# Kernel optimization log

Hardware: AMD Instinct MI355X
Metric: run time of the kernel (lower is better)

## Reference

```python
import jax, jax.numpy as jnp
import numpy as np

N, S, E = 8, 1024, 768
H = 12
D = E // H  # head_dim = 64
FF = 4 * E
EPS = 1e-5


def setup_inputs() -> dict:
    key = jax.random.key(0)
    ks = jax.random.split(key, 12)
    s = lambda fan_in: 1.0 / np.sqrt(fan_in)
    return {
        "x": jax.random.normal(ks[0], (N, S, E), dtype=jnp.float32),
        "ln1_g": jnp.ones((E,), jnp.float32),
        "ln1_b": jnp.zeros((E,), jnp.float32),
        "ln2_g": jnp.ones((E,), jnp.float32),
        "ln2_b": jnp.zeros((E,), jnp.float32),
        "w_attn": jax.random.normal(ks[1], (E, 3 * E), jnp.float32) * s(E),
        "b_attn": jax.random.normal(ks[2], (3 * E,), jnp.float32) * 0.02,
        "w_proj": jax.random.normal(ks[3], (E, E), jnp.float32) * s(E),
        "b_proj": jax.random.normal(ks[4], (E,), jnp.float32) * 0.02,
        "w_fc": jax.random.normal(ks[5], (E, FF), jnp.float32) * s(E),
        "b_fc": jax.random.normal(ks[6], (FF,), jnp.float32) * 0.02,
        "w_fc2": jax.random.normal(ks[7], (FF, E), jnp.float32) * s(FF),
        "b_fc2": jax.random.normal(ks[8], (E,), jnp.float32) * 0.02,
    }


def _layernorm(x, g, b):
    mu = jnp.mean(x, axis=-1, keepdims=True)
    var = jnp.var(x, axis=-1, keepdims=True)
    return (x - mu) * jax.lax.rsqrt(var + EPS) * g + b


def reference(x, ln1_g, ln1_b, ln2_g, ln2_b, w_attn, b_attn, w_proj, b_proj,
              w_fc, b_fc, w_fc2, b_fc2):
    # --- attention branch (pre-LN) ---
    h = _layernorm(x, ln1_g, ln1_b)
    qkv = h @ w_attn + b_attn                       # [N,S,3E]
    q, k, v = jnp.split(qkv, 3, axis=-1)
    q = q.reshape(N, S, H, D).transpose(0, 2, 1, 3)  # [N,H,S,D]
    k = k.reshape(N, S, H, D).transpose(0, 2, 1, 3)
    v = v.reshape(N, S, H, D).transpose(0, 2, 1, 3)
    attn = jnp.einsum('nhsd,nhtd->nhst', q, k) * (1.0 / np.sqrt(D))
    causal = jnp.tril(jnp.ones((S, S), bool))
    attn = jnp.where(causal, attn, -jnp.inf)
    p = jax.nn.softmax(attn, axis=-1)
    out = jnp.einsum('nhst,nhtd->nhsd', p, v)        # [N,H,S,D]
    out = out.transpose(0, 2, 1, 3).reshape(N, S, E)
    x = x + (out @ w_proj + b_proj)
    # --- MLP branch ---
    h2 = _layernorm(x, ln2_g, ln2_b)
    ff = jax.nn.gelu(h2 @ w_fc + b_fc, approximate=False)  # exact GELU (torch nn.GELU default)
    x = x + (ff @ w_fc2 + b_fc2)
    return x
```

## Files before the change

kernel.cpp:

```cpp
#include <hip/hip_runtime.h>
#include <hip/hip_bf16.h>
#include <stdint.h>

#define S_LEN 1024
#define E_DIM 768
#define H_N   12
#define FF_DIM 3072

typedef __hip_bfloat16 bf16;
using short8  = __attribute__((ext_vector_type(8))) short;
using short4v = __attribute__((ext_vector_type(4))) short;
using f32x4   = __attribute__((ext_vector_type(4))) float;

__device__ __forceinline__ void async_cp16(const void* g, void* l) {
  __builtin_amdgcn_global_load_lds(
      (__attribute__((address_space(1))) void*)(g),
      (__attribute__((address_space(3))) void*)(l), 16, 0, 0);
}

__global__ __launch_bounds__(256) void wcastT_all(
    const float* __restrict__ wa, const float* __restrict__ wp,
    const float* __restrict__ wf, const float* __restrict__ wf2,
    bf16* __restrict__ oa, bf16* __restrict__ op,
    bf16* __restrict__ of, bf16* __restrict__ of2) {
  __shared__ float t[32][33];
  int bid = blockIdx.x;
  const float* w; bf16* wt; int K, N, bx, by;
  if (bid < 1728)      { w = wa;  wt = oa;  K = 768;  N = 2304; int r = bid;        bx = r % 72; by = r / 72; }
  else if (bid < 2304) { w = wp;  wt = op;  K = 768;  N = 768;  int r = bid - 1728; bx = r % 24; by = r / 24; }
  else if (bid < 4608) { w = wf;  wt = of;  K = 768;  N = 3072; int r = bid - 2304; bx = r % 96; by = r / 96; }
  else                 { w = wf2; wt = of2; K = 3072; N = 768;  int r = bid - 4608; bx = r % 24; by = r / 24; }
  int x = threadIdx.x & 31;
  int y = threadIdx.x >> 5;
  for (int i = y; i < 32; i += 8)
    t[i][x] = w[(size_t)(by * 32 + i) * N + bx * 32 + x];
  __syncthreads();
  for (int i = y; i < 32; i += 8)
    wt[(size_t)(bx * 32 + i) * K + by * 32 + x] = __float2bfloat16(t[x][i]);
}

__global__ __launch_bounds__(256) void ln_rows(const float* __restrict__ x,
                                               const float* __restrict__ g,
                                               const float* __restrict__ b,
                                               bf16* __restrict__ out) {
  int row = blockIdx.x;
  int tid = threadIdx.x;
  const float* xr = x + (size_t)row * E_DIM;
  float v0 = xr[tid], v1 = xr[tid + 256], v2 = xr[tid + 512];
  float s = v0 + v1 + v2;
  float ss = v0 * v0 + v1 * v1 + v2 * v2;
  for (int o = 32; o > 0; o >>= 1) {
    s  += __shfl_down(s, o);
    ss += __shfl_down(ss, o);
  }
  __shared__ float ps[4], pq[4];
  int wv = tid >> 6;
  if ((tid & 63) == 0) { ps[wv] = s; pq[wv] = ss; }
  __syncthreads();
  s  = ps[0] + ps[1] + ps[2] + ps[3];
  ss = pq[0] + pq[1] + pq[2] + pq[3];
  float mu  = s * (1.0f / E_DIM);
  float var = ss * (1.0f / E_DIM) - mu * mu;
  float rs  = rsqrtf(var + 1e-5f);
  bf16* orow = out + (size_t)row * E_DIM;
  orow[tid]       = __float2bfloat16((v0 - mu) * rs * g[tid]       + b[tid]);
  orow[tid + 256] = __float2bfloat16((v1 - mu) * rs * g[tid + 256] + b[tid + 256]);
  orow[tid + 512] = __float2bfloat16((v2 - mu) * rs * g[tid + 512] + b[tid + 512]);
}

template <int MODE>
__global__ __launch_bounds__(512, 2) void gemm8(
    const bf16* __restrict__ A, const bf16* __restrict__ Bt,
    const float* __restrict__ bias,
    bf16* __restrict__ ob0, bf16* __restrict__ ob1, bf16* __restrict__ ob2,
    int M, int N, int K) {
  __shared__ bf16 lA[2][16384];
  __shared__ bf16 lB[2][16384];
  int tid = threadIdx.x;
  int w = tid >> 6, lane = tid & 63;
  int quad = lane >> 4, l16 = lane & 15;
  int wr = w >> 2, wc = w & 3;
  int gx = N >> 8;
  int flat = blockIdx.x;
  int y8 = flat & 7;
  int q2 = flat >> 3;
  int bx = q2 % gx;
  int by = (q2 / gx) * 8 + y8;
  int m0 = by << 8, n0 = bx << 8;

  f32x4 acc[8][4];
#pragma unroll
  for (int i = 0; i < 8; i++)
#pragma unroll
    for (int j = 0; j < 4; j++)
#pragma unroll
      for (int r = 0; r < 4; r++) acc[i][j][r] = 0.f;

  int xs = l16 & 7;
  int ko0 = (quad ^ xs) << 3;
  int ko1 = ((4 + quad) ^ xs) << 3;
  int sgo = ((tid & 7) ^ ((tid >> 3) & 7)) << 3;
  size_t aRB = (size_t)(m0 + (tid >> 3)) * K + sgo;
  size_t bRB = (size_t)(n0 + ((tid >> 8) << 6) + ((tid >> 3) & 31)) * K + sgo;
  int aD = tid * 8;
  int bD = ((tid >> 8) << 12) + (tid & 255) * 8;

  auto stA = [&](int buf, int mh, int kt) {
#pragma unroll
    for (int p = 0; p < 2; ++p)
      async_cp16(A + aRB + (size_t)(mh * 64 + p * 128) * K + (size_t)kt * 64,
                 &lA[buf][aD + mh * 4096 + p * 8192]);
  };
  auto stB = [&](int buf, int nh, int kt) {
#pragma unroll
    for (int p = 0; p < 2; ++p)
      async_cp16(Bt + bRB + (size_t)(nh * 32 + p * 128) * K + (size_t)kt * 64,
                 &lB[buf][bD + nh * 2048 + p * 8192]);
  };

  short8 af[4][2], b0f[2][2], b1f[2][2];

#define LD_A(BUF, MH)                                                      \
  {                                                                        \
    _Pragma("unroll") for (int i = 0; i < 4; ++i) {                        \
      const bf16* bp = &lA[BUF][(wr * 128 + (MH)*64 + i * 16 + l16) * 64]; \
      af[i][0] = *(const short8*)&bp[ko0];                                 \
      af[i][1] = *(const short8*)&bp[ko1];                                 \
    }                                                                      \
  }
#define LD_B(BUF, NH, DST)                                                 \
  {                                                                        \
    _Pragma("unroll") for (int j = 0; j < 2; ++j) {                        \
      const bf16* bp = &lB[BUF][(wc * 64 + (NH)*32 + j * 16 + l16) * 64];  \
      DST[j][0] = *(const short8*)&bp[ko0];                                \
      DST[j][1] = *(const short8*)&bp[ko1];                                \
    }                                                                      \
  }
#define DO_MFMA(MH, NH, BSRC)                                              \
  {                                                                        \
    __builtin_amdgcn_s_setprio(1);                                         \
    _Pragma("unroll") for (int ks = 0; ks < 2; ++ks)                       \
        _Pragma("unroll") for (int i = 0; i < 4; ++i)                      \
            _Pragma("unroll") for (int j = 0; j < 2; ++j)                  \
                acc[(MH)*4 + i][(NH)*2 + j] =                              \
        __builtin_amdgcn_mfma_f32_16x16x32_bf16(                           \
            BSRC[j][ks], af[i][ks], acc[(MH)*4 + i][(NH)*2 + j], 0, 0, 0); \
    __builtin_amdgcn_s_setprio(0);                                         \
  }
#define BAR() __builtin_amdgcn_s_barrier()
#define LGKM0() asm volatile("s_waitcnt lgkmcnt(0)" ::: "memory")
#define VM6() asm volatile("s_waitcnt vmcnt(6)" ::: "memory")
#define VM0() asm volatile("s_waitcnt vmcnt(0)" ::: "memory")

  stA(0, 0, 0); stA(0, 1, 0); stB(0, 0, 0); stB(0, 1, 0);
  stA(1, 0, 1); stB(1, 1, 1); stA(1, 1, 1);
  VM6();
  BAR();

  int nit = K >> 7;
  for (int it = 0; it < nit; ++it) {
    int kt1 = 2 * it + 1, ktA = 2 * it + 2, ktB = 2 * it + 3;
    bool more = (it + 1 < nit);
    LD_A(0, 0); LD_B(0, 0, b0f);
    stB(1, 0, kt1);
    BAR(); LGKM0(); DO_MFMA(0, 0, b0f); BAR();
    LD_B(0, 1, b1f);
    if (more) stA(0, 0, ktA);
    BAR(); LGKM0(); DO_MFMA(0, 1, b1f); BAR();
    LD_A(0, 1);
    if (more) stB(0, 1, ktA);
    BAR(); LGKM0(); DO_MFMA(1, 1, b1f); BAR();
    LD_B(0, 0, b0f);
    if (more) { stA(0, 1, ktA); VM6(); } else { VM0(); }
    BAR(); LGKM0(); DO_MFMA(1, 0, b0f); BAR();
    LD_A(1, 0); LD_B(1, 0, b0f);
    if (more) stB(0, 0, ktA);
    BAR(); LGKM0(); DO_MFMA(0, 0, b0f); BAR();
    LD_B(1, 1, b1f);
    if (more) stA(1, 0, ktB);
    BAR(); LGKM0(); DO_MFMA(0, 1, b1f); BAR();
    LD_A(1, 1);
    if (more) stB(1, 1, ktB);
    BAR(); LGKM0(); DO_MFMA(1, 1, b1f); BAR();
    LD_B(1, 0, b0f);
    if (more) { stA(1, 1, ktB); VM6(); }
    BAR(); LGKM0(); DO_MFMA(1, 0, b0f); BAR();
  }

#pragma unroll
  for (int nj = 0; nj < 4; ++nj) {
    int colb = n0 + wc * 64 + nj * 16 + quad * 4;
    f32x4 b4 = *(const f32x4*)&bias[colb];
#pragma unroll
    for (int mi = 0; mi < 8; ++mi) {
      int row = m0 + wr * 128 + mi * 16 + l16;
      f32x4 v = acc[mi][nj] + b4;
      if (MODE == 0) {
        int nn = row >> 10, s = row & 1023;
        if (colb < 768) {
          int h = colb >> 6, db = colb & 63;
          short4v pk;
          for (int r = 0; r < 4; r++)
            pk[r] = __builtin_bit_cast(short, __float2bfloat16(v[r] * 0.125f));
          *(short4v*)&ob0[(((size_t)nn * H_N + h) * S_LEN + s) * 64 + db] = pk;
        } else if (colb < 1536) {
          int c = colb - 768;
          size_t nh2 = (size_t)nn * H_N + (c >> 6);
          int d = c & 63;
          short4v pk;
          for (int r = 0; r < 4; r++)
            pk[r] = __builtin_bit_cast(short, __float2bfloat16(v[r]));
          *(short4v*)&ob1[((nh2 * 8 + (d >> 3)) * S_LEN + s) * 8 + (d & 7)] = pk;
        } else {
          int c = colb - 1536;
          size_t nh2 = (size_t)nn * H_N + (c >> 6);
          int d0 = c & 63;
          for (int r = 0; r < 4; r++)
            ob2[((nh2 * 128 + (s >> 3)) * 64 + d0 + r) * 8 + (s & 7)] =
                __float2bfloat16(v[r]);
        }
      } else if (MODE == 2) {
        short4v pk;
        for (int r = 0; r < 4; r++) {
          float x = v[r];
          float t = x * (1.59576912161f + 0.0713548162726f * x * x);
          float g = x * __builtin_amdgcn_rcpf(1.0f + __expf(-t));
          pk[r] = __builtin_bit_cast(short, __float2bfloat16(g));
        }
        *(short4v*)&ob0[(size_t)row * N + colb] = pk;
      }
    }
  }
#undef LD_A
#undef LD_B
#undef DO_MFMA
#undef BAR
#undef LGKM0
#undef VM6
#undef VM0
}

__global__ __launch_bounds__(256) void gemm_bt64(
    const bf16* __restrict__ A, const bf16* __restrict__ Bt,
    const float* __restrict__ bias, const float* __restrict__ resid,
    float* __restrict__ outf, int M, int N, int K) {
  __shared__ bf16 As[2][128 * 64];
  __shared__ bf16 Bs[2][64 * 64];
  int tid = threadIdx.x;
  int wave = tid >> 6, lane = tid & 63;
  int quad = lane >> 4, l16 = lane & 15;
  int gx = N >> 6;
  int flat = blockIdx.x;
  int y8 = flat & 7;
  int q2 = flat >> 3;
  int bx = q2 % gx;
  int by = (q2 / gx) * 8 + y8;
  int m0 = by * 128, n0 = bx * 64;
  int wm = wave * 32;
  f32x4 acc[2][4];
  for (int i = 0; i < 2; i++)
    for (int j = 0; j < 4; j++)
      for (int r = 0; r < 4; r++) acc[i][j][r] = 0.f;

  int xs = l16 & 7;
  int srow = tid >> 3;
  int scg = (((tid & 7) ^ (srow & 7)) << 3);
  const bf16* aptr = A  + (size_t)(m0 + srow) * K + scg;
  const bf16* bptr = Bt + (size_t)(n0 + srow) * K + scg;
  int ldst = tid * 8;

#pragma unroll
  for (int t = 0; t < 4; t++)
    async_cp16(aptr + (size_t)t * 32 * K, &As[0][ldst + t * 2048]);
#pragma unroll
  for (int t = 0; t < 2; t++)
    async_cp16(bptr + (size_t)t * 32 * K, &Bs[0][ldst + t * 2048]);

  int nkb = K >> 6;
  for (int ik = 0; ik < nkb; ++ik) {
    int cur = ik & 1;
    if (ik + 1 < nkb) {
      size_t ko = (size_t)(ik + 1) * 64;
#pragma unroll
      for (int t = 0; t < 4; t++)
        async_cp16(aptr + ko + (size_t)t * 32 * K, &As[cur ^ 1][ldst + t * 2048]);
#pragma unroll
      for (int t = 0; t < 2; t++)
        async_cp16(bptr + ko + (size_t)t * 32 * K, &Bs[cur ^ 1][ldst + t * 2048]);
      asm volatile("s_waitcnt vmcnt(6)" ::: "memory");
    } else {
      asm volatile("s_waitcnt vmcnt(0)" ::: "memory");
    }
    __builtin_amdgcn_s_barrier();
    asm volatile("" ::: "memory");
#pragma unroll
    for (int ks = 0; ks < 2; ks++) {
      int ko2 = (((ks * 4 + quad) ^ xs) << 3);
      short8 af[2], bfr[4];
      for (int i = 0; i < 2; i++)
        af[i] = *(const short8*)&As[cur][(wm + i * 16 + l16) * 64 + ko2];
      for (int j = 0; j < 4; j++)
        bfr[j] = *(const short8*)&Bs[cur][(j * 16 + l16) * 64 + ko2];
      for (int i = 0; i < 2; i++)
        for (int j = 0; j < 4; j++)
          acc[i][j] = __builtin_amdgcn_mfma_f32_16x16x32_bf16(
              bfr[j], af[i], acc[i][j], 0, 0, 0);
    }
    asm volatile("" ::: "memory");
    __builtin_amdgcn_s_barrier();
  }

  for (int j = 0; j < 4; j++) {
    int colb = n0 + j * 16 + quad * 4;
    f32x4 b4 = *(const f32x4*)&bias[colb];
    for (int i = 0; i < 2; i++) {
      int row = m0 + wm + i * 16 + l16;
      size_t idx = (size_t)row * N + colb;
      f32x4 rv = *(const f32x4*)&resid[idx];
      *(f32x4*)&outf[idx] = acc[i][j] + b4 + rv;
    }
  }
}

__global__ __launch_bounds__(256) void attn_fwd(
    const bf16* __restrict__ q, const bf16* __restrict__ kg,
    const bf16* __restrict__ vg, bf16* __restrict__ out) {
  __shared__ bf16 kt2[2][8 * 64 * 8];
  __shared__ bf16 vt2[2][8 * 64 * 8];
  __shared__ bf16 pba[4][16 * 68];
  __shared__ bf16 pbb[4][16 * 68];
  int flat = blockIdx.x;
  int xcd = flat & 7;
  int j = flat >> 3;
  int a = j & 7;
  int g = j >> 3;
  int nh = xcd * 12 + g;
  int b = 15 - a;
  int n = nh / H_N, h = nh % H_N;
  int tid = threadIdx.x, wave = tid >> 6, lane = tid & 63;
  int quad = lane >> 4, l16 = lane & 15;
  const bf16* qp = q  + (size_t)nh * S_LEN * 64;
  const bf16* kp = kg + (size_t)nh * 8 * S_LEN * 8;
  const bf16* vp = vg + (size_t)nh * 128 * 64 * 8;
  int qra = a * 64 + wave * 16;
  int qrb = b * 64 + wave * 16;

  short8 qfa[2], qfb[2];
  qfa[0] = *(const short8*)&qp[(size_t)(qra + l16) * 64 + quad * 8];
  qfa[1] = *(const short8*)&qp[(size_t)(qra + l16) * 64 + 32 + quad * 8];
  qfb[0] = *(const short8*)&qp[(size_t)(qrb + l16) * 64 + quad * 8];
  qfb[1] = *(const short8*)&qp[(size_t)(qrb + l16) * 64 + 32 + quad * 8];

  const bf16* kbase = kp + (((size_t)(tid >> 6) * S_LEN) + (tid & 63)) * 8;
  const bf16* vbase = vp + (((size_t)(tid >> 6) * 64) + (tid & 63)) * 8;

  f32x4 oaa[4], oab[4];
  for (int dt = 0; dt < 4; dt++)
    for (int r = 0; r < 4; r++) { oaa[dt][r] = 0.f; oab[dt][r] = 0.f; }
  float lia = 0.f, lib = 0.f;

  {
    bf16* lk = &kt2[0][0] + tid * 8;
    bf16* lv = &vt2[0][0] + tid * 8;
#pragma unroll
    for (int t = 0; t < 2; ++t) {
      async_cp16(kbase + (size_t)t * 4 * S_LEN * 8, lk + t * 2048);
      async_cp16(vbase + (size_t)t * 2048, lv + t * 2048);
    }
  }

  for (int kb = 0; kb <= b; ++kb) {
    bool act_a = (kb <= a);
    int cur = kb & 1;
    __syncthreads();

    short8 kf[2][4], vf[2][4];
#pragma unroll
    for (int ks = 0; ks < 2; ks++)
      for (int nt = 0; nt < 4; nt++) {
        kf[ks][nt] = *(const short8*)
            &kt2[cur][(size_t)((ks * 4 + quad) * 64 + nt * 16 + l16) * 8];
        vf[ks][nt] = *(const short8*)
            &vt2[cur][(size_t)((ks * 4 + quad) * 64 + nt * 16 + l16) * 8];
      }
    if (kb < b) {
      bf16* lk = &kt2[cur ^ 1][0] + tid * 8;
      bf16* lv = &vt2[cur ^ 1][0] + tid * 8;
      size_t kko = (size_t)(kb + 1) * 512;
      size_t vko = (size_t)(kb + 1) * 4096;
#pragma unroll
      for (int t = 0; t < 2; ++t) {
        async_cp16(kbase + kko + (size_t)t * 4 * S_LEN * 8, lk + t * 2048);
        async_cp16(vbase + vko + (size_t)t * 2048, lv + t * 2048);
      }
    }

    f32x4 sb4[4], sa4[4];
    for (int nt = 0; nt < 4; nt++) {
      for (int r = 0; r < 4; r++) { sb4[nt][r] = -10.f; sa4[nt][r] = -10.f; }
      for (int ks = 0; ks < 2; ks++) {
        sb4[nt] = __builtin_amdgcn_mfma_f32_16x16x32_bf16(kf[ks][nt], qfb[ks],
                                                          sb4[nt], 0, 0, 0);
        if (act_a)
          sa4[nt] = __builtin_amdgcn_mfma_f32_16x16x32_bf16(kf[ks][nt], qfa[ks],
                                                            sa4[nt], 0, 0, 0);
      }
    }
    if (kb == b) {
      int ql = wave * 16 + l16;
      for (int nt = 0; nt < 4; nt++)
        for (int r = 0; r < 4; r++)
          if (nt * 16 + quad * 4 + r > ql) sb4[nt][r] = -INFINITY;
    }
    if (kb == a) {
      int ql = wave * 16 + l16;
      for (int nt = 0; nt < 4; nt++)
        for (int r = 0; r < 4; r++)
          if (nt * 16 + quad * 4 + r > ql) sa4[nt][r] = -INFINITY;
    }

    float rsb = 0.f;
    for (int nt = 0; nt < 4; nt++)
      for (int r = 0; r < 4; r++) {
        float p = __expf(sb4[nt][r]);
        sb4[nt][r] = p;
        rsb += p;
      }
    rsb += __shfl_xor(rsb, 16);
    rsb += __shfl_xor(rsb, 32);
    lib += rsb;
    bf16* pwb = pbb[wave];
    for (int nt = 0; nt < 4; nt++) {
      short4v pk;
      for (int r = 0; r < 4; r++)
        pk[r] = __builtin_bit_cast(short, __float2bfloat16(sb4[nt][r]));
      *(short4v*)&pwb[l16 * 68 + nt * 16 + quad * 4] = pk;
    }
    if (act_a) {
      float rsa = 0.f;
      for (int nt = 0; nt < 4; nt++)
        for (int r = 0; r < 4; r++) {
          float p = __expf(sa4[nt][r]);
          sa4[nt][r] = p;
          rsa += p;
        }
      rsa += __shfl_xor(rsa, 16);
      rsa += __shfl_xor(rsa, 32);
      lia += rsa;
      bf16* pwa = pba[wave];
      for (int nt = 0; nt < 4; nt++) {
        short4v pk;
        for (int r = 0; r < 4; r++)
          pk[r] = __builtin_bit_cast(short, __float2bfloat16(sa4[nt][r]));
        *(short4v*)&pwa[l16 * 68 + nt * 16 + quad * 4] = pk;
      }
    }
    asm volatile("s_waitcnt lgkmcnt(0)" ::: "memory");

    for (int ks = 0; ks < 2; ks++) {
      short8 pfb = *(const short8*)&pbb[wave][l16 * 68 + ks * 32 + quad * 8];
      short8 pfa;
      if (act_a) pfa = *(const short8*)&pba[wave][l16 * 68 + ks * 32 + quad * 8];
      for (int dt = 0; dt < 4; dt++) {
        oab[dt] = __builtin_amdgcn_mfma_f32_16x16x32_bf16(vf[ks][dt], pfb,
                                                          oab[dt], 0, 0, 0);
        if (act_a)
          oaa[dt] = __builtin_amdgcn_mfma_f32_16x16x32_bf16(vf[ks][dt], pfa,
                                                            oaa[dt], 0, 0, 0);
      }
    }
  }

  float inva = 1.0f / lia, invb = 1.0f / lib;
  int ta = n * S_LEN + qra + l16;
  int tb = n * S_LEN + qrb + l16;
  for (int dt = 0; dt < 4; dt++) {
    short4v ova, ovb;
    for (int r = 0; r < 4; r++) {
      ova[r] = __builtin_bit_cast(short, __float2bfloat16(oaa[dt][r] * inva));
      ovb[r] = __builtin_bit_cast(short, __float2bfloat16(oab[dt][r] * invb));
    }
    *(short4v*)&out[(size_t)ta * E_DIM + h * 64 + dt * 16 + quad * 4] = ova;
    *(short4v*)&out[(size_t)tb * E_DIM + h * 64 + dt * 16 + quad * 4] = ovb;
  }
}

extern "C" void kernel_launch(void* const* d_in, const int* in_sizes, int n_in,
                              void* d_out, int out_size, void* d_ws, size_t ws_size,
                              hipStream_t stream) {
  (void)in_sizes; (void)n_in; (void)out_size; (void)ws_size;
  const float* x      = (const float*)d_in[0];
  const float* ln1_g  = (const float*)d_in[1];
  const float* ln1_b  = (const float*)d_in[2];
  const float* ln2_g  = (const float*)d_in[3];
  const float* ln2_b  = (const float*)d_in[4];
  const float* w_attn = (const float*)d_in[5];
  const float* b_attn = (const float*)d_in[6];
  const float* w_proj = (const float*)d_in[7];
  const float* b_proj = (const float*)d_in[8];
  const float* w_fc   = (const float*)d_in[9];
  const float* b_fc   = (const float*)d_in[10];
  const float* w_fc2  = (const float*)d_in[11];
  const float* b_fc2  = (const float*)d_in[12];
  float* out = (float*)d_out;

  char* ws = (char*)d_ws;
  bf16* wt_attn = (bf16*)(ws);
  bf16* wt_proj = (bf16*)(ws + 3538944);
  bf16* wt_fc   = (bf16*)(ws + 4718592);
  bf16* wt_fc2  = (bf16*)(ws + 9437184);
  bf16* hbuf    = (bf16*)(ws + 14155776);
  float* x2     = (float*)(ws + 26738688);
  bf16* qb      = (bf16*)(ws + 51904512);
  bf16* kbuf    = (bf16*)(ws + 64487424);
  bf16* vtb     = (bf16*)(ws + 77070336);
  bf16* ao      = (bf16*)(ws + 89653248);
  bf16* ff      = qb;

  dim3 blk(256);
  wcastT_all<<<dim3(6912), blk, 0, stream>>>(w_attn, w_proj, w_fc, w_fc2,
                                             wt_attn, wt_proj, wt_fc, wt_fc2);

  ln_rows<<<8192, blk, 0, stream>>>(x, ln1_g, ln1_b, hbuf);

  gemm8<0><<<dim3(288), dim3(512), 0, stream>>>(
      hbuf, wt_attn, b_attn, qb, kbuf, vtb, 8192, 2304, 768);

  attn_fwd<<<dim3(768), blk, 0, stream>>>(qb, kbuf, vtb, ao);

  gemm_bt64<<<dim3(12 * 64), blk, 0, stream>>>(
      ao, wt_proj, b_proj, x, x2, 8192, 768, 768);

  ln_rows<<<8192, blk, 0, stream>>>(x2, ln2_g, ln2_b, hbuf);

  gemm8<2><<<dim3(384), dim3(512), 0, stream>>>(
      hbuf, wt_fc, b_fc, ff, nullptr, nullptr, 8192, 3072, 768);

  gemm_bt64<<<dim3(12 * 64), blk, 0, stream>>>(
      ff, wt_fc2, b_fc2, x2, out, 8192, 768, 3072);
}
```

Before: 367.5 us.

## Write QKV GEMM output row-major and scatter V in separate kernel

The QKV GEMM epilogue now writes a plain row-major [tokens, 2304] bf16 buffer instead of scattering Q, K and V into per-head layouts. Attention reads Q and K straight from that strided buffer. A new scatter_v kernel rebuilds the blocked transposed V layout the attention kernel needs. The aim is to remove the scattered, partly scalar stores in the GEMM epilogue, at the cost of an extra kernel launch, an extra pass over V, and strided K/Q loads inside attention.

```diff
diff --git a/kernel.cpp b/kernel.cpp
--- a/kernel.cpp
+++ b/kernel.cpp
@@ -68,11 +68,26 @@
   orow[tid + 512] = __float2bfloat16((v2 - mu) * rs * g[tid + 512] + b[tid + 512]);
 }
 
+__global__ __launch_bounds__(256) void scatter_v(const bf16* __restrict__ qkv,
+                                                 bf16* __restrict__ vtb) {
+  int blk = blockIdx.x;
+  int n = blk >> 7, soct = blk & 127;
+  int tid = threadIdx.x;
+  for (int j = tid; j < 768; j += 256) {
+    int h = j >> 6, d = j & 63;
+    const bf16* src = qkv + ((size_t)(n * 1024 + soct * 8)) * 2304 + 1536 + h * 64 + d;
+    short8 v;
+#pragma unroll
+    for (int i = 0; i < 8; i++)
+      v[i] = __builtin_bit_cast(short, src[(size_t)i * 2304]);
+    *(short8*)&vtb[((((size_t)n * 12 + h) * 128 + soct) * 64 + d) * 8] = v;
+  }
+}
+
 template <int MODE>
 __global__ __launch_bounds__(512, 2) void gemm8(
     const bf16* __restrict__ A, const bf16* __restrict__ Bt,
-    const float* __restrict__ bias,
-    bf16* __restrict__ ob0, bf16* __restrict__ ob1, bf16* __restrict__ ob2,
+    const float* __restrict__ bias, bf16* __restrict__ outb,
     int M, int N, int K) {
   __shared__ bf16 lA[2][16384];
   __shared__ bf16 lB[2][16384];
@@ -191,44 +206,24 @@
   for (int nj = 0; nj < 4; ++nj) {
     int colb = n0 + wc * 64 + nj * 16 + quad * 4;
     f32x4 b4 = *(const f32x4*)&bias[colb];
+    float sc = (MODE == 1 && colb < 768) ? 0.125f : 1.0f;
 #pragma unroll
     for (int mi = 0; mi < 8; ++mi) {
       int row = m0 + wr * 128 + mi * 16 + l16;
       f32x4 v = acc[mi][nj] + b4;
-      if (MODE == 0) {
-        int nn = row >> 10, s = row & 1023;
-        if (colb < 768) {
-          int h = colb >> 6, db = colb & 63;
-          short4v pk;
-          for (int r = 0; r < 4; r++)
-            pk[r] = __builtin_bit_cast(short, __float2bfloat16(v[r] * 0.125f));
-          *(short4v*)&ob0[(((size_t)nn * H_N + h) * S_LEN + s) * 64 + db] = pk;
-        } else if (colb < 1536) {
-          int c = colb - 768;
-          size_t nh2 = (size_t)nn * H_N + (c >> 6);
-          int d = c & 63;
-          short4v pk;
-          for (int r = 0; r < 4; r++)
-            pk[r] = __builtin_bit_cast(short, __float2bfloat16(v[r]));
-          *(short4v*)&ob1[((nh2 * 8 + (d >> 3)) * S_LEN + s) * 8 + (d & 7)] = pk;
-        } else {
-          int c = colb - 1536;
-          size_t nh2 = (size_t)nn * H_N + (c >> 6);
-          int d0 = c & 63;
-          for (int r = 0; r < 4; r++)
-            ob2[((nh2 * 128 + (s >> 3)) * 64 + d0 + r) * 8 + (s & 7)] =
-                __float2bfloat16(v[r]);
-        }
-      } else if (MODE == 2) {
-        short4v pk;
+      short4v pk;
+      if (MODE == 1) {
+        for (int r = 0; r < 4; r++)
+          pk[r] = __builtin_bit_cast(short, __float2bfloat16(v[r] * sc));
+      } else {
         for (int r = 0; r < 4; r++) {
           float x = v[r];
           float t = x * (1.59576912161f + 0.0713548162726f * x * x);
           float g = x * __builtin_amdgcn_rcpf(1.0f + __expf(-t));
           pk[r] = __builtin_bit_cast(short, __float2bfloat16(g));
         }
-        *(short4v*)&ob0[(size_t)row * N + colb] = pk;
-      }
+      }
+      *(short4v*)&outb[(size_t)row * N + colb] = pk;
     }
   }
 #undef LD_A
@@ -323,8 +318,8 @@
 }
 
 __global__ __launch_bounds__(256) void attn_fwd(
-    const bf16* __restrict__ q, const bf16* __restrict__ kg,
-    const bf16* __restrict__ vg, bf16* __restrict__ out) {
+    const bf16* __restrict__ qkv, const bf16* __restrict__ vg,
+    bf16* __restrict__ out) {
   __shared__ bf16 kt2[2][8 * 64 * 8];
   __shared__ bf16 vt2[2][8 * 64 * 8];
   __shared__ bf16 pba[4][16 * 68];
@@ -339,19 +334,19 @@
   int n = nh / H_N, h = nh % H_N;
   int tid = threadIdx.x, wave = tid >> 6, lane = tid & 63;
   int quad = lane >> 4, l16 = lane & 15;
-  const bf16* qp = q  + (size_t)nh * S_LEN * 64;
-  const bf16* kp = kg + (size_t)nh * 8 * S_LEN * 8;
+  const bf16* qp = qkv + (size_t)n * S_LEN * 2304 + (size_t)h * 64;
   const bf16* vp = vg + (size_t)nh * 128 * 64 * 8;
   int qra = a * 64 + wave * 16;
   int qrb = b * 64 + wave * 16;
 
   short8 qfa[2], qfb[2];
-  qfa[0] = *(const short8*)&qp[(size_t)(qra + l16) * 64 + quad * 8];
-  qfa[1] = *(const short8*)&qp[(size_t)(qra + l16) * 64 + 32 + quad * 8];
-  qfb[0] = *(const short8*)&qp[(size_t)(qrb + l16) * 64 + quad * 8];
-  qfb[1] = *(const short8*)&qp[(size_t)(qrb + l16) * 64 + 32 + quad * 8];
-
-  const bf16* kbase = kp + (((size_t)(tid >> 6) * S_LEN) + (tid & 63)) * 8;
+  qfa[0] = *(const short8*)&qp[(size_t)(qra + l16) * 2304 + quad * 8];
+  qfa[1] = *(const short8*)&qp[(size_t)(qra + l16) * 2304 + 32 + quad * 8];
+  qfb[0] = *(const short8*)&qp[(size_t)(qrb + l16) * 2304 + quad * 8];
+  qfb[1] = *(const short8*)&qp[(size_t)(qrb + l16) * 2304 + 32 + quad * 8];
+
+  const bf16* kbase = qkv + ((size_t)n * S_LEN + (tid & 63)) * 2304 + 768 +
+                      h * 64 + ((tid >> 6) << 3);
   const bf16* vbase = vp + (((size_t)(tid >> 6) * 64) + (tid & 63)) * 8;
 
   f32x4 oaa[4], oab[4];
@@ -364,7 +359,7 @@
     bf16* lv = &vt2[0][0] + tid * 8;
 #pragma unroll
     for (int t = 0; t < 2; ++t) {
-      async_cp16(kbase + (size_t)t * 4 * S_LEN * 8, lk + t * 2048);
+      async_cp16(kbase + t * 32, lk + t * 2048);
       async_cp16(vbase + (size_t)t * 2048, lv + t * 2048);
     }
   }
@@ -386,11 +381,11 @@
     if (kb < b) {
       bf16* lk = &kt2[cur ^ 1][0] + tid * 8;
       bf16* lv = &vt2[cur ^ 1][0] + tid * 8;
-      size_t kko = (size_t)(kb + 1) * 512;
+      size_t kko = (size_t)(kb + 1) * 64 * 2304;
       size_t vko = (size_t)(kb + 1) * 4096;
 #pragma unroll
       for (int t = 0; t < 2; ++t) {
-        async_cp16(kbase + kko + (size_t)t * 4 * S_LEN * 8, lk + t * 2048);
+        async_cp16(kbase + kko + t * 32, lk + t * 2048);
         async_cp16(vbase + vko + (size_t)t * 2048, lv + t * 2048);
       }
     }
@@ -511,11 +506,10 @@
   bf16* wt_fc2  = (bf16*)(ws + 9437184);
   bf16* hbuf    = (bf16*)(ws + 14155776);
   float* x2     = (float*)(ws + 26738688);
-  bf16* qb      = (bf16*)(ws + 51904512);
-  bf16* kbuf    = (bf16*)(ws + 64487424);
-  bf16* vtb     = (bf16*)(ws + 77070336);
-  bf16* ao      = (bf16*)(ws + 89653248);
-  bf16* ff      = qb;
+  bf16* qkvb    = (bf16*)(ws + 51904512);
+  bf16* vtb     = (bf16*)(ws + 89653248);
+  bf16* ao      = hbuf;
+  bf16* ff      = qkvb;
 
   dim3 blk(256);
   wcastT_all<<<dim3(6912), blk, 0, stream>>>(w_attn, w_proj, w_fc, w_fc2,
@@ -523,10 +517,12 @@
 
   ln_rows<<<8192, blk, 0, stream>>>(x, ln1_g, ln1_b, hbuf);
 
-  gemm8<0><<<dim3(288), dim3(512), 0, stream>>>(
-      hbuf, wt_attn, b_attn, qb, kbuf, vtb, 8192, 2304, 768);
-
-  attn_fwd<<<dim3(768), blk, 0, stream>>>(qb, kbuf, vtb, ao);
+  gemm8<1><<<dim3(288), dim3(512), 0, stream>>>(
+      hbuf, wt_attn, b_attn, qkvb, 8192, 2304, 768);
+
+  scatter_v<<<dim3(1024), blk, 0, stream>>>(qkvb, vtb);
+
+  attn_fwd<<<dim3(768), blk, 0, stream>>>(qkvb, vtb, ao);
 
   gemm_bt64<<<dim3(12 * 64), blk, 0, stream>>>(
       ao, wt_proj, b_proj, x, x2, 8192, 768, 768);
@@ -534,7 +530,7 @@
   ln_rows<<<8192, blk, 0, stream>>>(x2, ln2_g, ln2_b, hbuf);
 
   gemm8<2><<<dim3(384), dim3(512), 0, stream>>>(
-      hbuf, wt_fc, b_fc, ff, nullptr, nullptr, 8192, 3072, 768);
+      hbuf, wt_fc, b_fc, ff, 8192, 3072, 768);
 
   gemm_bt64<<<dim3(12 * 64), blk, 0, stream>>>(
       ff, wt_fc2, b_fc2, x2, out, 8192, 768, 3072);
```

New measurement: 378.7 us. 3.1% more time.
